# Performance work log

Hardware: AMD Instinct MI355X
Metric: run time of the kernel (lower is better)

Reference implementation:

```python
import jax, jax.numpy as jnp
import numpy as np

MOMENTUM = 0.99
EPS = 1e-08


def setup_inputs() -> dict:
    key = jax.random.key(0)
    k1, = jax.random.split(key, 1)
    B, F, T = 32, 257, 3000
    mag = jax.random.uniform(k1, (B, F, T), dtype=jnp.float32)  # magnitudes >= 0
    bias = jnp.zeros((1,), dtype=jnp.float32)
    running_mean = jnp.ones((1,), dtype=jnp.float32)
    return {"mag": mag, "bias": bias, "running_mean": running_mean}


def reference(mag, bias, running_mean):
    """Causal per-frame EMA energy normalization (eval-mode sequence path).

    mag: [B, F, T] -> (mag_norm [B, F, T], mag_mean [B, 1, T])
    """
    B, F, T = mag.shape
    frame_means = mag.mean(axis=1)          # [B, T]
    init = jnp.broadcast_to(running_mean, (B,))  # m_0 = running_mean per batch

    def step(carry, fm_t):
        m = MOMENTUM * carry + (1.0 - MOMENTUM) * fm_t  # [B]
        return m, m

    _, means = jax.lax.scan(step, init, frame_means.T)  # means: [T, B]
    mean_with_bias = means.T + bias[0]                  # [B, T]
    mag_norm = mag / (mean_with_bias[:, None, :] + EPS)  # [B, F, T]
    mag_mean = mean_with_bias[:, None, :]               # [B, 1, T]
    return mag_norm, mag_mean
```

## Files before the change

kernel.cpp:

```cpp
#include <hip/hip_runtime.h>


#define B_   32
#define F_   257
#define T_   3000
#define T4   750
#define NG1  16
#define MOM  0.99f
#define OMM  0.01f
#define EPS_ 1e-8f
#define INVF (1.0f / 257.0f)

#define ACC4(a, v) { a.x += v.x; a.y += v.y; a.z += v.z; a.w += v.w; }

__global__ __launch_bounds__(256) void k1_partial(const float* __restrict__ mag,
                                                  float* __restrict__ partial) {
    const int blk = blockIdx.x;
    const int b   = blk >> 4;
    const int g   = blk & 15;
    const int tid = threadIdx.x;
    const bool has2 = tid < (T4 - 512);

    const float4* magv = reinterpret_cast<const float4*>(mag)
                       + ((size_t)(b * F_ + g * 16)) * T4;
    float4 a0 = make_float4(0.f,0.f,0.f,0.f);
    float4 a1 = make_float4(0.f,0.f,0.f,0.f);
    float4 a2 = make_float4(0.f,0.f,0.f,0.f);

    #pragma unroll 4
    for (int r = 0; r < 16; ++r) {
        const float4* row = magv + (size_t)r * T4;
        float4 v0 = row[tid];
        float4 v1 = row[tid + 256];
        ACC4(a0, v0);
        ACC4(a1, v1);
        if (has2) { float4 v2 = row[tid + 512]; ACC4(a2, v2); }
    }
    if (g == 15) {
        const float4* row = magv + (size_t)16 * T4;
        float4 v0 = row[tid];
        float4 v1 = row[tid + 256];
        ACC4(a0, v0);
        ACC4(a1, v1);
        if (has2) { float4 v2 = row[tid + 512]; ACC4(a2, v2); }
    }

    float4* pv = reinterpret_cast<float4*>(partial) + (size_t)blk * T4;
    pv[tid]       = a0;
    pv[tid + 256] = a1;
    if (has2) pv[tid + 512] = a2;
}

__global__ __launch_bounds__(256) void k2_scan_norm(
    const float* __restrict__ partial,
    const float* __restrict__ bias,
    const float* __restrict__ rmean,
    const float* __restrict__ mag,
    float* __restrict__ out,
    float* __restrict__ mag_mean)
{
    __shared__ float4 xs4[T4];
    float* xs = reinterpret_cast<float*>(xs4);
    __shared__ float sA[256];
    __shared__ float sB[256];

    const int blk = blockIdx.x;
    const int b   = blk / 33;
    const int ch  = blk % 33;
    const int tid = threadIdx.x;
    const bool c2 = tid < (T4 - 512);

    {
        const float4* pv = reinterpret_cast<const float4*>(partial)
                         + (size_t)b * NG1 * T4;
        float4 s0 = make_float4(0.f,0.f,0.f,0.f);
        float4 s1 = make_float4(0.f,0.f,0.f,0.f);
        float4 s2 = make_float4(0.f,0.f,0.f,0.f);
        #pragma unroll 4
        for (int r = 0; r < NG1; ++r) {
            const float4* rp = pv + (size_t)r * T4;
            float4 v0 = rp[tid];
            float4 v1 = rp[tid + 256];
            ACC4(s0, v0);
            ACC4(s1, v1);
            if (c2) { float4 v2 = rp[tid + 512]; ACC4(s2, v2); }
        }
        s0.x *= INVF; s0.y *= INVF; s0.z *= INVF; s0.w *= INVF;
        s1.x *= INVF; s1.y *= INVF; s1.z *= INVF; s1.w *= INVF;
        xs4[tid]       = s0;
        xs4[tid + 256] = s1;
        if (c2) {
            s2.x *= INVF; s2.y *= INVF; s2.z *= INVF; s2.w *= INVF;
            xs4[tid + 512] = s2;
        }
    }
    __syncthreads();

    const int CH = 12;
    const int t0 = tid * CH;
    float A = 1.f, Bv = 0.f;
    if (t0 < T_) {
        #pragma unroll
        for (int j = 0; j < CH; ++j) {
            Bv = MOM * Bv + OMM * xs[t0 + j];
            A *= MOM;
        }
    }
    sA[tid] = A; sB[tid] = Bv;
    __syncthreads();

    for (int off = 1; off < 256; off <<= 1) {
        float cA = sA[tid], cB = sB[tid];
        float pA = 1.f, pB = 0.f;
        if (tid >= off) { pA = sA[tid - off]; pB = sB[tid - off]; }
        __syncthreads();
        if (tid >= off) { sA[tid] = pA * cA; sB[tid] = pB * cA + cB; }
        __syncthreads();
    }
    float pA = 1.f, pB = 0.f;
    if (tid > 0) { pA = sA[tid - 1]; pB = sB[tid - 1]; }
    __syncthreads();

    const float bias0 = bias[0];
    if (t0 < T_) {
        float m = pA * rmean[0] + pB;
        #pragma unroll
        for (int j = 0; j < CH; ++j) {
            m = MOM * m + OMM * xs[t0 + j];
            xs[t0 + j] = m + bias0;
        }
    }
    __syncthreads();

    if (ch == 0) {
        float4* mmv = reinterpret_cast<float4*>(mag_mean) + (size_t)b * T4;
        for (int i = tid; i < T4; i += 256) mmv[i] = xs4[i];
    }
    for (int i = tid; i < T4; i += 256) {
        float4 v = xs4[i];
        v.x = 1.0f / (v.x + EPS_); v.y = 1.0f / (v.y + EPS_);
        v.z = 1.0f / (v.z + EPS_); v.w = 1.0f / (v.w + EPS_);
        xs4[i] = v;
    }
    __syncthreads();

    const float4 r0 = xs4[tid];
    const float4 r1 = xs4[tid + 256];
    const float4 r2 = c2 ? xs4[tid + 512] : r0;

    const int f0 = ch * 8;
    const int nr = (ch == 32) ? 1 : 8;
    const float4* magv = reinterpret_cast<const float4*>(mag)
                       + ((size_t)(b * F_ + f0)) * T4;
    float4* ov = reinterpret_cast<float4*>(out)
               + ((size_t)(b * F_ + f0)) * T4;

    for (int r = 0; r < nr; ++r) {
        const float4* row  = magv + (size_t)r * T4;
        float4*       orow = ov   + (size_t)r * T4;
        float4 v0 = row[tid];
        float4 v1 = row[tid + 256];
        float4 o;
        o.x = v0.x * r0.x; o.y = v0.y * r0.y; o.z = v0.z * r0.z; o.w = v0.w * r0.w;
        orow[tid] = o;
        o.x = v1.x * r1.x; o.y = v1.y * r1.y; o.z = v1.z * r1.z; o.w = v1.w * r1.w;
        orow[tid + 256] = o;
        if (c2) {
            float4 v2 = row[tid + 512];
            o.x = v2.x * r2.x; o.y = v2.y * r2.y; o.z = v2.z * r2.z; o.w = v2.w * r2.w;
            orow[tid + 512] = o;
        }
    }
}

__global__ __launch_bounds__(256) void k_reduce_scan(const float* __restrict__ src,
                                                     int nrows,
                                                     const float* __restrict__ bias,
                                                     const float* __restrict__ rmean,
                                                     float* __restrict__ recip,
                                                     float* __restrict__ mag_mean) {
    __shared__ float4 xs4[T4];
    float* xs = reinterpret_cast<float*>(xs4);
    __shared__ float sA[256];
    __shared__ float sB[256];

    const int b   = blockIdx.x;
    const int tid = threadIdx.x;
    const bool has2 = tid < (T4 - 512);

    {
        const float4* sv = reinterpret_cast<const float4*>(src)
                         + (size_t)b * nrows * T4;
        float4 a0 = make_float4(0.f,0.f,0.f,0.f);
        float4 a1 = make_float4(0.f,0.f,0.f,0.f);
        float4 a2 = make_float4(0.f,0.f,0.f,0.f);
        #pragma unroll 4
        for (int r = 0; r < nrows; ++r) {
            const float4* row = sv + (size_t)r * T4;
            float4 v0 = row[tid];
            float4 v1 = row[tid + 256];
            ACC4(a0, v0); ACC4(a1, v1);
            if (has2) { float4 v2 = row[tid + 512]; ACC4(a2, v2); }
        }
        a0.x *= INVF; a0.y *= INVF; a0.z *= INVF; a0.w *= INVF;
        a1.x *= INVF; a1.y *= INVF; a1.z *= INVF; a1.w *= INVF;
        xs4[tid]       = a0;
        xs4[tid + 256] = a1;
        if (has2) {
            a2.x *= INVF; a2.y *= INVF; a2.z *= INVF; a2.w *= INVF;
            xs4[tid + 512] = a2;
        }
    }
    __syncthreads();

    const int CH = 12;
    const int t0 = tid * CH;
    float A = 1.f, Bv = 0.f;
    if (t0 < T_) {
        #pragma unroll
        for (int j = 0; j < CH; ++j) {
            Bv = MOM * Bv + OMM * xs[t0 + j];
            A *= MOM;
        }
    }
    sA[tid] = A; sB[tid] = Bv;
    __syncthreads();

    for (int off = 1; off < 256; off <<= 1) {
        float cA = sA[tid], cB = sB[tid];
        float pA = 1.f, pB = 0.f;
        if (tid >= off) { pA = sA[tid - off]; pB = sB[tid - off]; }
        __syncthreads();
        if (tid >= off) { sA[tid] = pA * cA; sB[tid] = pB * cA + cB; }
        __syncthreads();
    }
    float pA = 1.f, pB = 0.f;
    if (tid > 0) { pA = sA[tid - 1]; pB = sB[tid - 1]; }
    __syncthreads();

    const float bias0 = bias[0];
    if (t0 < T_) {
        float m = pA * rmean[0] + pB;
        #pragma unroll
        for (int j = 0; j < CH; ++j) {
            m = MOM * m + OMM * xs[t0 + j];
            xs[t0 + j] = m + bias0;
        }
    }
    __syncthreads();

    float4* mmv = reinterpret_cast<float4*>(mag_mean) + (size_t)b * T4;
    float4* rcv = reinterpret_cast<float4*>(recip)    + (size_t)b * T4;
    for (int i = tid; i < T4; i += 256) {
        float4 v = xs4[i];
        mmv[i] = v;
        float4 rv;
        rv.x = 1.0f / (v.x + EPS_); rv.y = 1.0f / (v.y + EPS_);
        rv.z = 1.0f / (v.z + EPS_); rv.w = 1.0f / (v.w + EPS_);
        rcv[i] = rv;
    }
}

__global__ __launch_bounds__(256) void k3_norm(const float* __restrict__ mag,
                                               const float* __restrict__ recip,
                                               float* __restrict__ out) {
    __shared__ float4 rec4[T4];
    const int blk = blockIdx.x;
    const int b   = blk / 33;
    const int ch  = blk % 33;
    const int tid = threadIdx.x;

    {
        const float4* rcv = reinterpret_cast<const float4*>(recip) + (size_t)b * T4;
        for (int i = tid; i < T4; i += 256) rec4[i] = rcv[i];
    }
    __syncthreads();

    const bool has2 = tid < (T4 - 512);
    const float4 r0 = rec4[tid];
    const float4 r1 = rec4[tid + 256];
    const float4 r2 = has2 ? rec4[tid + 512] : r0;

    const int f0 = ch * 8;
    const int nr = (ch == 32) ? 1 : 8;
    const float4* magv = reinterpret_cast<const float4*>(mag)
                       + ((size_t)(b * F_ + f0)) * T4;
    float4* ov = reinterpret_cast<float4*>(out)
               + ((size_t)(b * F_ + f0)) * T4;

    for (int r = 0; r < nr; ++r) {
        const float4* row  = magv + (size_t)r * T4;
        float4*       orow = ov   + (size_t)r * T4;
        float4 v0 = row[tid];
        float4 v1 = row[tid + 256];
        float4 o;
        o.x = v0.x * r0.x; o.y = v0.y * r0.y; o.z = v0.z * r0.z; o.w = v0.w * r0.w;
        orow[tid] = o;
        o.x = v1.x * r1.x; o.y = v1.y * r1.y; o.z = v1.z * r1.z; o.w = v1.w * r1.w;
        orow[tid + 256] = o;
        if (has2) {
            float4 v2 = row[tid + 512];
            o.x = v2.x * r2.x; o.y = v2.y * r2.y; o.z = v2.z * r2.z; o.w = v2.w * r2.w;
            orow[tid + 512] = o;
        }
    }
}

extern "C" void kernel_launch(void* const* d_in, const int* in_sizes, int n_in,
                              void* d_out, int out_size, void* d_ws, size_t ws_size,
                              hipStream_t stream) {
    (void)in_sizes; (void)n_in; (void)out_size;
    const float* mag   = (const float*)d_in[0];
    const float* bias  = (const float*)d_in[1];
    const float* rmean = (const float*)d_in[2];
    float* out      = (float*)d_out;
    float* mag_mean = out + (size_t)B_ * F_ * T_;

    const size_t partial_sz = (size_t)B_ * NG1 * T_ * sizeof(float);
    const size_t recip_sz   = (size_t)B_ * T_ * sizeof(float);

    if (ws_size >= partial_sz) {
        float* partial = (float*)d_ws;
        k1_partial<<<B_ * NG1, 256, 0, stream>>>(mag, partial);
        k2_scan_norm<<<B_ * 33, 256, 0, stream>>>(partial, bias, rmean, mag,
                                                  out, mag_mean);
    } else {
        float* recip = (float*)d_ws;
        k_reduce_scan<<<B_, 256, 0, stream>>>(mag, F_, bias, rmean,
                                              recip, mag_mean);
        k3_norm<<<B_ * 33, 256, 0, stream>>>(mag, recip, out);
    }
}
```

Baseline: 207.1 us.

## Fuse reduce, scan and normalize into one cooperative kernel with grid syncs

Replaces the two-kernel path with a single cooperative kernel of 1024 blocks. Each block reduces its 8-row feature slab into a partial, then after a grid sync 32 blocks compute the frame means, run the EMA scan and write reciprocals. After a second grid sync every block normalizes the same slab it reduced, which aims to reuse mag from L2/infinity cache and save a launch. The cost is two grid-wide barriers, a serial scan phase where only 32 blocks work, and a dependence on cooperative launch support with the old path kept as a fallback.

```diff
diff --git a/kernel.cpp b/kernel.cpp
--- a/kernel.cpp
+++ b/kernel.cpp
@@ -1,11 +1,14 @@
 #include <hip/hip_runtime.h>
+#include <hip/hip_cooperative_groups.h>
+
+namespace cg = cooperative_groups;
 
 
 #define B_   32
 #define F_   257
 #define T_   3000
 #define T4   750
-#define NG1  16
+#define NCH  32
 #define MOM  0.99f
 #define OMM  0.01f
 #define EPS_ 1e-8f
@@ -13,71 +16,61 @@
 
 #define ACC4(a, v) { a.x += v.x; a.y += v.y; a.z += v.z; a.w += v.w; }
 
-__global__ __launch_bounds__(256) void k1_partial(const float* __restrict__ mag,
-                                                  float* __restrict__ partial) {
-    const int blk = blockIdx.x;
-    const int b   = blk >> 4;
-    const int g   = blk & 15;
-    const int tid = threadIdx.x;
-    const bool has2 = tid < (T4 - 512);
-
-    const float4* magv = reinterpret_cast<const float4*>(mag)
-                       + ((size_t)(b * F_ + g * 16)) * T4;
-    float4 a0 = make_float4(0.f,0.f,0.f,0.f);
-    float4 a1 = make_float4(0.f,0.f,0.f,0.f);
-    float4 a2 = make_float4(0.f,0.f,0.f,0.f);
-
-    #pragma unroll 4
-    for (int r = 0; r < 16; ++r) {
-        const float4* row = magv + (size_t)r * T4;
-        float4 v0 = row[tid];
-        float4 v1 = row[tid + 256];
-        ACC4(a0, v0);
-        ACC4(a1, v1);
-        if (has2) { float4 v2 = row[tid + 512]; ACC4(a2, v2); }
-    }
-    if (g == 15) {
-        const float4* row = magv + (size_t)16 * T4;
-        float4 v0 = row[tid];
-        float4 v1 = row[tid + 256];
-        ACC4(a0, v0);
-        ACC4(a1, v1);
-        if (has2) { float4 v2 = row[tid + 512]; ACC4(a2, v2); }
-    }
-
-    float4* pv = reinterpret_cast<float4*>(partial) + (size_t)blk * T4;
-    pv[tid]       = a0;
-    pv[tid + 256] = a1;
-    if (has2) pv[tid + 512] = a2;
-}
-
-__global__ __launch_bounds__(256) void k2_scan_norm(
-    const float* __restrict__ partial,
+__global__ __launch_bounds__(256, 4) void ema_coop(
+    const float* __restrict__ mag,
     const float* __restrict__ bias,
     const float* __restrict__ rmean,
-    const float* __restrict__ mag,
     float* __restrict__ out,
-    float* __restrict__ mag_mean)
+    float* __restrict__ mag_mean,
+    float* __restrict__ partial,
+    float* __restrict__ recip)
 {
     __shared__ float4 xs4[T4];
     float* xs = reinterpret_cast<float*>(xs4);
     __shared__ float sA[256];
     __shared__ float sB[256];
 
+    cg::grid_group grid = cg::this_grid();
+
     const int blk = blockIdx.x;
-    const int b   = blk / 33;
-    const int ch  = blk % 33;
+    const int b   = blk >> 5;
+    const int ch  = blk & (NCH - 1);
     const int tid = threadIdx.x;
     const bool c2 = tid < (T4 - 512);
 
+    const float4* magv = reinterpret_cast<const float4*>(mag)
+                       + (size_t)(b * F_ + ch * 8) * T4;
+    const int nr = (ch == NCH - 1) ? 9 : 8;
+
     {
+        float4 a0 = make_float4(0.f,0.f,0.f,0.f);
+        float4 a1 = make_float4(0.f,0.f,0.f,0.f);
+        float4 a2 = make_float4(0.f,0.f,0.f,0.f);
+        for (int r = 0; r < nr; ++r) {
+            const float4* row = magv + (size_t)r * T4;
+            float4 v0 = row[tid];
+            float4 v1 = row[tid + 256];
+            ACC4(a0, v0);
+            ACC4(a1, v1);
+            if (c2) { float4 v2 = row[tid + 512]; ACC4(a2, v2); }
+        }
+        float4* pv = reinterpret_cast<float4*>(partial) + (size_t)blk * T4;
+        pv[tid]       = a0;
+        pv[tid + 256] = a1;
+        if (c2) pv[tid + 512] = a2;
+    }
+    __threadfence();
+    grid.sync();
+
+    if (blk < B_) {
+        const int sb = blk;
         const float4* pv = reinterpret_cast<const float4*>(partial)
-                         + (size_t)b * NG1 * T4;
+                         + (size_t)sb * NCH * T4;
         float4 s0 = make_float4(0.f,0.f,0.f,0.f);
         float4 s1 = make_float4(0.f,0.f,0.f,0.f);
         float4 s2 = make_float4(0.f,0.f,0.f,0.f);
         #pragma unroll 4
-        for (int r = 0; r < NG1; ++r) {
+        for (int r = 0; r < NCH; ++r) {
             const float4* rp = pv + (size_t)r * T4;
             float4 v0 = rp[tid];
             float4 v1 = rp[tid + 256];
@@ -93,68 +86,64 @@
             s2.x *= INVF; s2.y *= INVF; s2.z *= INVF; s2.w *= INVF;
             xs4[tid + 512] = s2;
         }
-    }
-    __syncthreads();
-
-    const int CH = 12;
-    const int t0 = tid * CH;
-    float A = 1.f, Bv = 0.f;
-    if (t0 < T_) {
-        #pragma unroll
-        for (int j = 0; j < CH; ++j) {
-            Bv = MOM * Bv + OMM * xs[t0 + j];
-            A *= MOM;
-        }
-    }
-    sA[tid] = A; sB[tid] = Bv;
-    __syncthreads();
-
-    for (int off = 1; off < 256; off <<= 1) {
-        float cA = sA[tid], cB = sB[tid];
+        __syncthreads();
+
+        const int CH = 12;
+        const int t0 = tid * CH;
+        float A = 1.f, Bv = 0.f;
+        if (t0 < T_) {
+            #pragma unroll
+            for (int j = 0; j < CH; ++j) {
+                Bv = MOM * Bv + OMM * xs[t0 + j];
+                A *= MOM;
+            }
+        }
+        sA[tid] = A; sB[tid] = Bv;
+        __syncthreads();
+
+        for (int off = 1; off < 256; off <<= 1) {
+            float cA = sA[tid], cB = sB[tid];
+            float pA = 1.f, pB = 0.f;
+            if (tid >= off) { pA = sA[tid - off]; pB = sB[tid - off]; }
+            __syncthreads();
+            if (tid >= off) { sA[tid] = pA * cA; sB[tid] = pB * cA + cB; }
+            __syncthreads();
+        }
         float pA = 1.f, pB = 0.f;
-        if (tid >= off) { pA = sA[tid - off]; pB = sB[tid - off]; }
-        __syncthreads();
-        if (tid >= off) { sA[tid] = pA * cA; sB[tid] = pB * cA + cB; }
-        __syncthreads();
-    }
-    float pA = 1.f, pB = 0.f;
-    if (tid > 0) { pA = sA[tid - 1]; pB = sB[tid - 1]; }
-    __syncthreads();
-
-    const float bias0 = bias[0];
-    if (t0 < T_) {
-        float m = pA * rmean[0] + pB;
-        #pragma unroll
-        for (int j = 0; j < CH; ++j) {
-            m = MOM * m + OMM * xs[t0 + j];
-            xs[t0 + j] = m + bias0;
-        }
-    }
-    __syncthreads();
-
-    if (ch == 0) {
-        float4* mmv = reinterpret_cast<float4*>(mag_mean) + (size_t)b * T4;
-        for (int i = tid; i < T4; i += 256) mmv[i] = xs4[i];
-    }
-    for (int i = tid; i < T4; i += 256) {
-        float4 v = xs4[i];
-        v.x = 1.0f / (v.x + EPS_); v.y = 1.0f / (v.y + EPS_);
-        v.z = 1.0f / (v.z + EPS_); v.w = 1.0f / (v.w + EPS_);
-        xs4[i] = v;
-    }
-    __syncthreads();
-
-    const float4 r0 = xs4[tid];
-    const float4 r1 = xs4[tid + 256];
-    const float4 r2 = c2 ? xs4[tid + 512] : r0;
-
-    const int f0 = ch * 8;
-    const int nr = (ch == 32) ? 1 : 8;
-    const float4* magv = reinterpret_cast<const float4*>(mag)
-                       + ((size_t)(b * F_ + f0)) * T4;
-    float4* ov = reinterpret_cast<float4*>(out)
-               + ((size_t)(b * F_ + f0)) * T4;
-
+        if (tid > 0) { pA = sA[tid - 1]; pB = sB[tid - 1]; }
+        __syncthreads();
+
+        const float bias0 = bias[0];
+        if (t0 < T_) {
+            float m = pA * rmean[0] + pB;
+            #pragma unroll
+            for (int j = 0; j < CH; ++j) {
+                m = MOM * m + OMM * xs[t0 + j];
+                xs[t0 + j] = m + bias0;
+            }
+        }
+        __syncthreads();
+
+        float4* mmv = reinterpret_cast<float4*>(mag_mean) + (size_t)sb * T4;
+        float4* rcv = reinterpret_cast<float4*>(recip)    + (size_t)sb * T4;
+        for (int i = tid; i < T4; i += 256) {
+            float4 v = xs4[i];
+            mmv[i] = v;
+            float4 rv;
+            rv.x = 1.0f / (v.x + EPS_); rv.y = 1.0f / (v.y + EPS_);
+            rv.z = 1.0f / (v.z + EPS_); rv.w = 1.0f / (v.w + EPS_);
+            rcv[i] = rv;
+        }
+        __threadfence();
+    }
+    grid.sync();
+
+    const float4* rcv = reinterpret_cast<const float4*>(recip) + (size_t)b * T4;
+    const float4 r0 = rcv[tid];
+    const float4 r1 = rcv[tid + 256];
+    const float4 r2 = c2 ? rcv[tid + 512] : r0;
+
+    float4* ov = reinterpret_cast<float4*>(out) + (size_t)(b * F_ + ch * 8) * T4;
     for (int r = 0; r < nr; ++r) {
         const float4* row  = magv + (size_t)r * T4;
         float4*       orow = ov   + (size_t)r * T4;
@@ -173,42 +162,83 @@
     }
 }
 
-__global__ __launch_bounds__(256) void k_reduce_scan(const float* __restrict__ src,
-                                                     int nrows,
-                                                     const float* __restrict__ bias,
-                                                     const float* __restrict__ rmean,
-                                                     float* __restrict__ recip,
-                                                     float* __restrict__ mag_mean) {
+#define NG1  16
+
+__global__ __launch_bounds__(256) void k1_partial(const float* __restrict__ mag,
+                                                  float* __restrict__ partial) {
+    const int blk = blockIdx.x;
+    const int b   = blk >> 4;
+    const int g   = blk & 15;
+    const int tid = threadIdx.x;
+    const bool has2 = tid < (T4 - 512);
+
+    const float4* magv = reinterpret_cast<const float4*>(mag)
+                       + ((size_t)(b * F_ + g * 16)) * T4;
+    float4 a0 = make_float4(0.f,0.f,0.f,0.f);
+    float4 a1 = make_float4(0.f,0.f,0.f,0.f);
+    float4 a2 = make_float4(0.f,0.f,0.f,0.f);
+
+    #pragma unroll 4
+    for (int r = 0; r < 16; ++r) {
+        const float4* row = magv + (size_t)r * T4;
+        float4 v0 = row[tid];
+        float4 v1 = row[tid + 256];
+        ACC4(a0, v0); ACC4(a1, v1);
+        if (has2) { float4 v2 = row[tid + 512]; ACC4(a2, v2); }
+    }
+    if (g == 15) {
+        const float4* row = magv + (size_t)16 * T4;
+        float4 v0 = row[tid];
+        float4 v1 = row[tid + 256];
+        ACC4(a0, v0); ACC4(a1, v1);
+        if (has2) { float4 v2 = row[tid + 512]; ACC4(a2, v2); }
+    }
+    float4* pv = reinterpret_cast<float4*>(partial) + (size_t)blk * T4;
+    pv[tid]       = a0;
+    pv[tid + 256] = a1;
+    if (has2) pv[tid + 512] = a2;
+}
+
+__global__ __launch_bounds__(256) void k2_scan_norm(
+    const float* __restrict__ partial,
+    const float* __restrict__ bias,
+    const float* __restrict__ rmean,
+    const float* __restrict__ mag,
+    float* __restrict__ out,
+    float* __restrict__ mag_mean)
+{
     __shared__ float4 xs4[T4];
     float* xs = reinterpret_cast<float*>(xs4);
     __shared__ float sA[256];
     __shared__ float sB[256];
 
-    const int b   = blockIdx.x;
+    const int blk = blockIdx.x;
+    const int b   = blk / 33;
+    const int ch  = blk % 33;
     const int tid = threadIdx.x;
-    const bool has2 = tid < (T4 - 512);
+    const bool c2 = tid < (T4 - 512);
 
     {
-        const float4* sv = reinterpret_cast<const float4*>(src)
-                         + (size_t)b * nrows * T4;
-        float4 a0 = make_float4(0.f,0.f,0.f,0.f);
-        float4 a1 = make_float4(0.f,0.f,0.f,0.f);
-        float4 a2 = make_float4(0.f,0.f,0.f,0.f);
+        const float4* pv = reinterpret_cast<const float4*>(partial)
+                         + (size_t)b * NG1 * T4;
+        float4 s0 = make_float4(0.f,0.f,0.f,0.f);
+        float4 s1 = make_float4(0.f,0.f,0.f,0.f);
+        float4 s2 = make_float4(0.f,0.f,0.f,0.f);
         #pragma unroll 4
-        for (int r = 0; r < nrows; ++r) {
-            const float4* row = sv + (size_t)r * T4;
-            float4 v0 = row[tid];
-            float4 v1 = row[tid + 256];
-            ACC4(a0, v0); ACC4(a1, v1);
-            if (has2) { float4 v2 = row[tid + 512]; ACC4(a2, v2); }
-        }
-        a0.x *= INVF; a0.y *= INVF; a0.z *= INVF; a0.w *= INVF;
-        a1.x *= INVF; a1.y *= INVF; a1.z *= INVF; a1.w *= INVF;
-        xs4[tid]       = a0;
-        xs4[tid + 256] = a1;
-        if (has2) {
-            a2.x *= INVF; a2.y *= INVF; a2.z *= INVF; a2.w *= INVF;
-            xs4[tid + 512] = a2;
+        for (int r = 0; r < NG1; ++r) {
+            const float4* rp = pv + (size_t)r * T4;
+            float4 v0 = rp[tid];
+            float4 v1 = rp[tid + 256];
+            ACC4(s0, v0); ACC4(s1, v1);
+            if (c2) { float4 v2 = rp[tid + 512]; ACC4(s2, v2); }
+        }
+        s0.x *= INVF; s0.y *= INVF; s0.z *= INVF; s0.w *= INVF;
+        s1.x *= INVF; s1.y *= INVF; s1.z *= INVF; s1.w *= INVF;
+        xs4[tid]       = s0;
+        xs4[tid + 256] = s1;
+        if (c2) {
+            s2.x *= INVF; s2.y *= INVF; s2.z *= INVF; s2.w *= INVF;
+            xs4[tid + 512] = s2;
         }
     }
     __syncthreads();
@@ -249,37 +279,21 @@
     }
     __syncthreads();
 
-    float4* mmv = reinterpret_cast<float4*>(mag_mean) + (size_t)b * T4;
-    float4* rcv = reinterpret_cast<float4*>(recip)    + (size_t)b * T4;
+    if (ch == 0) {
+        float4* mmv = reinterpret_cast<float4*>(mag_mean) + (size_t)b * T4;
+        for (int i = tid; i < T4; i += 256) mmv[i] = xs4[i];
+    }
     for (int i = tid; i < T4; i += 256) {
         float4 v = xs4[i];
-        mmv[i] = v;
-        float4 rv;
-        rv.x = 1.0f / (v.x + EPS_); rv.y = 1.0f / (v.y + EPS_);
-        rv.z = 1.0f / (v.z + EPS_); rv.w = 1.0f / (v.w + EPS_);
-        rcv[i] = rv;
-    }
-}
-
-__global__ __launch_bounds__(256) void k3_norm(const float* __restrict__ mag,
-                                               const float* __restrict__ recip,
-                                               float* __restrict__ out) {
-    __shared__ float4 rec4[T4];
-    const int blk = blockIdx.x;
-    const int b   = blk / 33;
-    const int ch  = blk % 33;
-    const int tid = threadIdx.x;
-
-    {
-        const float4* rcv = reinterpret_cast<const float4*>(recip) + (size_t)b * T4;
-        for (int i = tid; i < T4; i += 256) rec4[i] = rcv[i];
-    }
-    __syncthreads();
-
-    const bool has2 = tid < (T4 - 512);
-    const float4 r0 = rec4[tid];
-    const float4 r1 = rec4[tid + 256];
-    const float4 r2 = has2 ? rec4[tid + 512] : r0;
+        v.x = 1.0f / (v.x + EPS_); v.y = 1.0f / (v.y + EPS_);
+        v.z = 1.0f / (v.z + EPS_); v.w = 1.0f / (v.w + EPS_);
+        xs4[i] = v;
+    }
+    __syncthreads();
+
+    const float4 r0 = xs4[tid];
+    const float4 r1 = xs4[tid + 256];
+    const float4 r2 = c2 ? xs4[tid + 512] : r0;
 
     const int f0 = ch * 8;
     const int nr = (ch == 32) ? 1 : 8;
@@ -298,7 +312,7 @@
         orow[tid] = o;
         o.x = v1.x * r1.x; o.y = v1.y * r1.y; o.z = v1.z * r1.z; o.w = v1.w * r1.w;
         orow[tid + 256] = o;
-        if (has2) {
+        if (c2) {
             float4 v2 = row[tid + 512];
             o.x = v2.x * r2.x; o.y = v2.y * r2.y; o.z = v2.z * r2.z; o.w = v2.w * r2.w;
             orow[tid + 512] = o;
@@ -316,18 +330,35 @@
     float* out      = (float*)d_out;
     float* mag_mean = out + (size_t)B_ * F_ * T_;
 
+    const size_t coop_partial = (size_t)B_ * NCH * T_;
+    const size_t coop_recip   = (size_t)B_ * T_;
+    const size_t need_coop    = (coop_partial + coop_recip) * sizeof(float);
+
+    static int coop_ok = -1;
+    if (coop_ok < 0) {
+        int dev = 0, val = 0;
+        hipGetDevice(&dev);
+        hipDeviceGetAttribute(&val, hipDeviceAttributeCooperativeLaunch, dev);
+        coop_ok = val ? 1 : 0;
+    }
+
+    if (coop_ok == 1 && ws_size >= need_coop) {
+        float* partial = (float*)d_ws;
+        float* recip   = partial + coop_partial;
+        void* args[] = { (void*)&mag, (void*)&bias, (void*)&rmean,
+                         (void*)&out, (void*)&mag_mean,
+                         (void*)&partial, (void*)&recip };
+        hipError_t e = hipLaunchCooperativeKernel((const void*)ema_coop,
+                                                  dim3(B_ * NCH), dim3(256),
+                                                  args, 0, stream);
+        if (e == hipSuccess) return;
+        coop_ok = 0;
+    }
+
     const size_t partial_sz = (size_t)B_ * NG1 * T_ * sizeof(float);
-    const size_t recip_sz   = (size_t)B_ * T_ * sizeof(float);
-
-    if (ws_size >= partial_sz) {
-        float* partial = (float*)d_ws;
-        k1_partial<<<B_ * NG1, 256, 0, stream>>>(mag, partial);
-        k2_scan_norm<<<B_ * 33, 256, 0, stream>>>(partial, bias, rmean, mag,
-                                                  out, mag_mean);
-    } else {
-        float* recip = (float*)d_ws;
-        k_reduce_scan<<<B_, 256, 0, stream>>>(mag, F_, bias, rmean,
-                                              recip, mag_mean);
-        k3_norm<<<B_ * 33, 256, 0, stream>>>(mag, recip, out);
-    }
+    float* partial = (float*)d_ws;
+    k1_partial<<<B_ * NG1, 256, 0, stream>>>(mag, partial);
+    k2_scan_norm<<<B_ * 33, 256, 0, stream>>>(partial, bias, rmean, mag,
+                                              out, mag_mean);
+    (void)partial_sz;
 }
```

Measured after the change: 465.3 us. 125% more time.
